# Performance work log

Hardware: AMD Instinct MI355X
Metric: run time of the kernel (lower is better)

## Reference

```python
import jax, jax.numpy as jnp
import numpy as np

N_NODES = 100000
N_RAND_EDGES = 1600000
NEG_SLOPE = 0.2


def setup_inputs() -> dict:
    key = jax.random.key(0)
    ks = jax.random.split(key, 12)
    X = jax.random.normal(ks[0], (N_NODES, 1433), dtype=jnp.float32)
    src_r = jax.random.randint(ks[1], (N_RAND_EDGES,), 0, N_NODES)
    dst_r = jax.random.randint(ks[2], (N_RAND_EDGES,), 0, N_NODES)
    loops = jnp.arange(N_NODES, dtype=src_r.dtype)
    src = jnp.concatenate([src_r, loops])  # [E] self loops ensure in-degree >= 1
    dst = jnp.concatenate([dst_r, loops])
    s0 = 1.0 / np.sqrt(1433.0)
    s1 = 1.0 / np.sqrt(140.0)
    W0 = jax.random.normal(ks[3], (1433, 140), jnp.float32) * s0
    al0 = jax.random.normal(ks[4], (140,), jnp.float32) * s1
    ar0 = jax.random.normal(ks[5], (140,), jnp.float32) * s1
    b0 = jnp.zeros((140,), jnp.float32)
    W1 = jax.random.normal(ks[6], (140, 7), jnp.float32) * s1
    al1 = jax.random.normal(ks[7], (7,), jnp.float32) * 0.3
    ar1 = jax.random.normal(ks[8], (7,), jnp.float32) * 0.3
    b1 = jnp.zeros((7,), jnp.float32)
    return dict(X=X, src=src, dst=dst, W0=W0, al0=al0, ar0=ar0, b0=b0,
                W1=W1, al1=al1, ar1=ar1, b1=b1)


def gat_layer(X, src, dst, W, al, ar, b):
    """One single-head DGL GATConv: proj -> edge attn -> edge softmax -> scatter -> bias -> ReLU."""
    n = X.shape[0]
    h = X @ W                      # [N, d_out]
    el = h @ al                    # [N] src attention term
    er = h @ ar                    # [N] dst attention term
    e = jax.nn.leaky_relu(el[src] + er[dst], NEG_SLOPE)   # [E]
    # segment softmax over incoming edges of each dst node
    m = jax.ops.segment_max(e, dst, num_segments=n)       # [N]
    ex = jnp.exp(e - m[dst])                              # [E]
    denom = jax.ops.segment_sum(ex, dst, num_segments=n)  # [N]
    a = ex / denom[dst]                                   # [E]
    msg = h[src] * a[:, None]                             # [E, d_out]
    out = jax.ops.segment_sum(msg, dst, num_segments=n)   # [N, d_out]
    return jax.nn.relu(out + b)


def reference(X, src, dst, W0, al0, ar0, b0, W1, al1, ar1, b1):
    h1 = gat_layer(X, src, dst, W0, al0, ar0, b0)   # [N, 140]
    h2 = gat_layer(h1, src, dst, W1, al1, ar1, b1)  # [N, 7]
    return h2
```

## Files before the change

kernel.cpp:

```cpp
#include <hip/hip_runtime.h>
#include <hip/hip_bf16.h>

typedef __bf16 bf16x8 __attribute__((ext_vector_type(8)));
typedef float f32x4 __attribute__((ext_vector_type(4)));
typedef unsigned short u16x8 __attribute__((ext_vector_type(8)));
typedef unsigned short ushort_t;

#define GK 1433
#define GN 140
#define NP 144
#define KT 45

__device__ __forceinline__ ushort_t f2bf_trunc(float v) {
    return (ushort_t)(__builtin_bit_cast(unsigned int, v) >> 16);
}
__device__ __forceinline__ ushort_t f2bf_rne(float v) {
    unsigned int u = __builtin_bit_cast(unsigned int, v);
    unsigned int r = u + 0x7fffu + ((u >> 16) & 1u);
    return (ushort_t)(r >> 16);
}
__device__ __forceinline__ float bf2f(unsigned int u16) {
    return __builtin_bit_cast(float, u16 << 16);
}

__global__ void k_wpack(const float* __restrict__ W0, ushort_t* __restrict__ Wp) {
    int i = blockIdx.x * 256 + threadIdx.x;
    if (i >= KT * 9 * 64) return;
    int lane = i & 63, tile = i >> 6;
    int kt = tile / 9, nt = tile - kt * 9;
    int n = nt * 16 + (lane & 15);
    int kb = kt * 32 + (lane >> 4) * 8;
    u16x8 v;
#pragma unroll
    for (int j = 0; j < 8; ++j) {
        int k = kb + j;
        v[j] = (k < GK && n < GN) ? f2bf_trunc(W0[k * GN + n]) : (ushort_t)0;
    }
    ((u16x8*)Wp)[i] = v;
}

__global__ __launch_bounds__(256) void k_gemm0(const float* __restrict__ X,
                                               const ushort_t* __restrict__ Wp,
                                               ushort_t* __restrict__ h0p, int M) {
    const int lane = threadIdx.x & 63;
    const int wave = threadIdx.x >> 6;
    const int m = lane & 15;
    const int q = lane >> 4;
    const int rowbase = blockIdx.x * 128 + wave * 32;

    f32x4 acc[2][9];
#pragma unroll
    for (int i = 0; i < 2; ++i)
#pragma unroll
        for (int j = 0; j < 9; ++j) acc[i][j] = (f32x4){0.f, 0.f, 0.f, 0.f};

    int r0 = rowbase + m;      if (r0 > M - 1) r0 = M - 1;
    int r1 = rowbase + 16 + m; if (r1 > M - 1) r1 = M - 1;
    const float* x0 = X + (size_t)r0 * GK;
    const float* x1 = X + (size_t)r1 * GK;
    const u16x8* wq = (const u16x8*)Wp;

    for (int kt = 0; kt < KT; ++kt) {
        const int kb = kt * 32 + q * 8;
        u16x8 t0, t1;
        if (kb + 8 <= GK) {
#pragma unroll
            for (int j = 0; j < 8; ++j) {
                t0[j] = f2bf_trunc(x0[kb + j]);
                t1[j] = f2bf_trunc(x1[kb + j]);
            }
        } else {
#pragma unroll
            for (int j = 0; j < 8; ++j) {
                int k = kb + j;
                t0[j] = (k < GK) ? f2bf_trunc(x0[k]) : (ushort_t)0;
                t1[j] = (k < GK) ? f2bf_trunc(x1[k]) : (ushort_t)0;
            }
        }
        bf16x8 a0 = __builtin_bit_cast(bf16x8, t0);
        bf16x8 a1 = __builtin_bit_cast(bf16x8, t1);
#pragma unroll
        for (int nt = 0; nt < 9; ++nt) {
            bf16x8 b = __builtin_bit_cast(bf16x8, wq[((kt * 9 + nt) << 6) + lane]);
            acc[0][nt] = __builtin_amdgcn_mfma_f32_16x16x32_bf16(a0, b, acc[0][nt], 0, 0, 0);
            acc[1][nt] = __builtin_amdgcn_mfma_f32_16x16x32_bf16(a1, b, acc[1][nt], 0, 0, 0);
        }
    }
#pragma unroll
    for (int mf = 0; mf < 2; ++mf)
#pragma unroll
        for (int reg = 0; reg < 4; ++reg) {
            int r = rowbase + mf * 16 + q * 4 + reg;
            if (r < M) {
                ushort_t* orow = h0p + (size_t)r * NP + m;
#pragma unroll
                for (int nt = 0; nt < 9; ++nt) orow[nt * 16] = f2bf_rne(acc[mf][nt][reg]);
            }
        }
}

__global__ __launch_bounds__(256) void k_elr0(const ushort_t* __restrict__ h0p,
                                              const float* __restrict__ al,
                                              const float* __restrict__ ar,
                                              float* __restrict__ el, float* __restrict__ er, int N) {
    __shared__ float als[NP], ars[NP];
    for (int i = threadIdx.x; i < NP; i += 256) {
        als[i] = (i < GN) ? al[i] : 0.f;
        ars[i] = (i < GN) ? ar[i] : 0.f;
    }
    __syncthreads();
    int node = blockIdx.x * 256 + threadIdx.x;
    if (node >= N) return;
    const unsigned int* row = (const unsigned int*)(h0p + (size_t)node * NP);
    float e1 = 0.f, e2 = 0.f;
#pragma unroll 4
    for (int f = 0; f < NP / 2; ++f) {
        unsigned int p = row[f];
        float v0 = bf2f(p & 0xffffu), v1 = bf2f(p >> 16);
        e1 += v0 * als[2 * f] + v1 * als[2 * f + 1];
        e2 += v0 * ars[2 * f] + v1 * ars[2 * f + 1];
    }
    el[node] = e1;
    er[node] = e2;
}

__global__ void k_hist(const int* __restrict__ dst, int E, int* __restrict__ counts) {
    int i = blockIdx.x * 256 + threadIdx.x;
    if (i < E) atomicAdd(&counts[dst[i]], 1);
}

__global__ void k_scan_block(const int* __restrict__ in, int n, int* __restrict__ part, int* __restrict__ bsum) {
    __shared__ int sh[256];
    int t = threadIdx.x, i = blockIdx.x * 256 + t;
    int v = (i < n) ? in[i] : 0;
    sh[t] = v;
    __syncthreads();
    for (int off = 1; off < 256; off <<= 1) {
        int add = (t >= off) ? sh[t - off] : 0;
        __syncthreads();
        sh[t] += add;
        __syncthreads();
    }
    if (i < n) part[i] = sh[t] - v;
    if (t == 255) bsum[blockIdx.x] = sh[255];
}

__global__ void k_scan_single(const int* __restrict__ in, int n, int* __restrict__ out) {
    __shared__ int sh[512];
    int t = threadIdx.x;
    int v = (t < n) ? in[t] : 0;
    sh[t] = v;
    __syncthreads();
    for (int off = 1; off < 512; off <<= 1) {
        int add = (t >= off) ? sh[t - off] : 0;
        __syncthreads();
        sh[t] += add;
        __syncthreads();
    }
    if (t < n) out[t] = sh[t] - v;
}

__global__ void k_offsets(const int* __restrict__ part, const int* __restrict__ bscan,
                          int N, int E, int* __restrict__ offsets) {
    int i = blockIdx.x * 256 + threadIdx.x;
    if (i < N) offsets[i] = part[i] + bscan[i >> 8];
    if (i == 0) offsets[N] = E;
}

__global__ void k_fill(const int* __restrict__ src, const int* __restrict__ dst, int E,
                       const int* __restrict__ offsets, int* __restrict__ cursor, int* __restrict__ eidx) {
    int i = blockIdx.x * 256 + threadIdx.x;
    if (i < E) {
        int d = dst[i];
        int p = atomicAdd(&cursor[d], 1);
        eidx[offsets[d] + p] = src[i];
    }
}

__device__ __forceinline__ float leaky(float x) { return (x > 0.f) ? x : 0.2f * x; }

__global__ __launch_bounds__(256) void k_agg0(const ushort_t* __restrict__ h0p,
                                              const float* __restrict__ el, const float* __restrict__ er,
                                              const int* __restrict__ offsets, const int* __restrict__ eidx,
                                              const float* __restrict__ b0,
                                              const float* __restrict__ W1,
                                              const float* __restrict__ al1,
                                              const float* __restrict__ ar1,
                                              float* __restrict__ h1p, float* __restrict__ el1,
                                              float* __restrict__ er1, int N) {
    __shared__ float W1s[NP * 8];
    __shared__ float b0s[NP];
    __shared__ float al1s[8], ar1s[8];
    int t = threadIdx.x;
    for (int i = t; i < NP * 8; i += 256) {
        int f = i >> 3, k = i & 7;
        W1s[i] = (f < GN && k < 7) ? W1[f * 7 + k] : 0.f;
    }
    for (int i = t; i < NP; i += 256) b0s[i] = (i < GN) ? b0[i] : 0.f;
    if (t < 8) {
        al1s[t] = (t < 7) ? al1[t] : 0.f;
        ar1s[t] = (t < 7) ? ar1[t] : 0.f;
    }
    __syncthreads();

    int node = blockIdx.x * 4 + (t >> 6);
    if (node >= N) return;
    int lane = t & 63;
    int s0 = offsets[node], s1 = offsets[node + 1];
    float erd = er[node];

    float mm = -1e30f;
    for (int j = s0 + lane; j < s1; j += 64) mm = fmaxf(mm, leaky(el[eidx[j]] + erd));
#pragma unroll
    for (int o = 1; o < 64; o <<= 1) mm = fmaxf(mm, __shfl_xor(mm, o));

    float dn = 0.f;
    for (int j = s0 + lane; j < s1; j += 64) dn += __expf(leaky(el[eidx[j]] + erd) - mm);
#pragma unroll
    for (int o = 1; o < 64; o <<= 1) dn += __shfl_xor(dn, o);
    float inv = 1.f / dn;

    float a0 = 0.f, a1 = 0.f, a2 = 0.f, a3 = 0.f;
    for (int j = s0; j < s1; ++j) {
        int s = eidx[j];
        float w = __expf(leaky(el[s] + erd) - mm) * inv;
        const unsigned int* hr = (const unsigned int*)(h0p + (size_t)s * NP);
        unsigned int pp = hr[lane];
        a0 += w * bf2f(pp & 0xffffu);
        a1 += w * bf2f(pp >> 16);
        if (lane < 8) {
            unsigned int pe = hr[64 + lane];
            a2 += w * bf2f(pe & 0xffffu);
            a3 += w * bf2f(pe >> 16);
        }
    }
    int f0 = 2 * lane, f1 = 2 * lane + 1;
    float h10 = fmaxf(a0 + b0s[f0], 0.f);
    float h11 = fmaxf(a1 + b0s[f1], 0.f);
    float h12 = 0.f, h13 = 0.f;
    if (lane < 8) {
        h12 = fmaxf(a2 + b0s[128 + 2 * lane], 0.f);
        h13 = fmaxf(a3 + b0s[129 + 2 * lane], 0.f);
    }

    float p[7];
#pragma unroll
    for (int k = 0; k < 7; ++k) {
        float v = h10 * W1s[f0 * 8 + k] + h11 * W1s[f1 * 8 + k];
        if (lane < 8) v += h12 * W1s[(128 + 2 * lane) * 8 + k] + h13 * W1s[(129 + 2 * lane) * 8 + k];
#pragma unroll
        for (int o = 1; o < 64; o <<= 1) v += __shfl_xor(v, o);
        p[k] = v;
    }
    if (lane == 0) {
        float e1 = 0.f, e2 = 0.f;
        float* hp = h1p + (size_t)node * 8;
#pragma unroll
        for (int k = 0; k < 7; ++k) {
            hp[k] = p[k];
            e1 += p[k] * al1s[k];
            e2 += p[k] * ar1s[k];
        }
        hp[7] = 0.f;
        el1[node] = e1;
        er1[node] = e2;
    }
}

__global__ __launch_bounds__(256) void k_agg1(const float* __restrict__ h1p,
                                              const float* __restrict__ el, const float* __restrict__ er,
                                              const int* __restrict__ offsets, const int* __restrict__ eidx,
                                              const float* __restrict__ b1,
                                              float* __restrict__ out, int N) {
    int t = threadIdx.x;
    int node = blockIdx.x * 4 + (t >> 6);
    if (node >= N) return;
    int lane = t & 63;
    int s0 = offsets[node], s1 = offsets[node + 1];
    float erd = er[node];

    float mm = -1e30f;
    for (int j = s0 + lane; j < s1; j += 64) mm = fmaxf(mm, leaky(el[eidx[j]] + erd));
#pragma unroll
    for (int o = 1; o < 64; o <<= 1) mm = fmaxf(mm, __shfl_xor(mm, o));

    float dn = 0.f;
    for (int j = s0 + lane; j < s1; j += 64) dn += __expf(leaky(el[eidx[j]] + erd) - mm);
#pragma unroll
    for (int o = 1; o < 64; o <<= 1) dn += __shfl_xor(dn, o);
    float inv = 1.f / dn;

    float acc[7] = {0.f, 0.f, 0.f, 0.f, 0.f, 0.f, 0.f};
    for (int j = s0 + lane; j < s1; j += 64) {
        int s = eidx[j];
        float w = __expf(leaky(el[s] + erd) - mm) * inv;
        const float4* hp = (const float4*)(h1p + (size_t)s * 8);
        float4 q0 = hp[0], q1 = hp[1];
        acc[0] += w * q0.x; acc[1] += w * q0.y; acc[2] += w * q0.z; acc[3] += w * q0.w;
        acc[4] += w * q1.x; acc[5] += w * q1.y; acc[6] += w * q1.z;
    }
#pragma unroll
    for (int k = 0; k < 7; ++k)
#pragma unroll
        for (int o = 1; o < 64; o <<= 1) acc[k] += __shfl_xor(acc[k], o);

    if (lane == 0) {
        float* orow = out + (size_t)node * 7;
#pragma unroll
        for (int k = 0; k < 7; ++k)
            orow[k] = fmaxf(acc[k] + b1[k], 0.f);
    }
}

extern "C" void kernel_launch(void* const* d_in, const int* in_sizes, int n_in,
                              void* d_out, int out_size, void* d_ws, size_t ws_size,
                              hipStream_t stream) {
    const float* X = (const float*)d_in[0];
    const int* src = (const int*)d_in[1];
    const int* dst = (const int*)d_in[2];
    const float* W0 = (const float*)d_in[3];
    const float* al0 = (const float*)d_in[4];
    const float* ar0 = (const float*)d_in[5];
    const float* b0 = (const float*)d_in[6];
    const float* W1 = (const float*)d_in[7];
    const float* al1 = (const float*)d_in[8];
    const float* ar1 = (const float*)d_in[9];
    const float* b1 = (const float*)d_in[10];
    float* out = (float*)d_out;

    const int N = in_sizes[0] / GK;
    const int E = in_sizes[1];

    char* w = (char*)d_ws;
    auto alloc = [&](size_t bytes) {
        char* p = w;
        w += (bytes + 255) & ~(size_t)255;
        return p;
    };
    ushort_t* wpack = (ushort_t*)alloc((size_t)KT * 9 * 64 * 8 * 2);
    ushort_t* h0p = (ushort_t*)alloc((size_t)N * NP * 2);
    float* el0 = (float*)alloc((size_t)N * 4);
    float* er0 = (float*)alloc((size_t)N * 4);
    int* counts = (int*)alloc(2 * (size_t)N * 4);
    int* cursor = counts + N;
    int* part = (int*)alloc((size_t)N * 4);
    int* bsum = (int*)alloc(512 * 4);
    int* bscan = (int*)alloc(512 * 4);
    int* offsets = (int*)alloc(((size_t)N + 1) * 4);
    int* eidx = (int*)alloc((size_t)E * 4);
    float* h1p = (float*)alloc((size_t)N * 8 * 4);
    float* el1 = (float*)alloc((size_t)N * 4);
    float* er1 = (float*)alloc((size_t)N * 4);

    hipMemsetAsync(counts, 0, 2 * (size_t)N * sizeof(int), stream);

    k_wpack<<<(KT * 9 * 64 + 255) / 256, 256, 0, stream>>>(W0, wpack);
    k_gemm0<<<(N + 127) / 128, 256, 0, stream>>>(X, wpack, h0p, N);
    k_elr0<<<(N + 255) / 256, 256, 0, stream>>>(h0p, al0, ar0, el0, er0, N);

    int nb = (N + 255) / 256;
    k_hist<<<(E + 255) / 256, 256, 0, stream>>>(dst, E, counts);
    k_scan_block<<<nb, 256, 0, stream>>>(counts, N, part, bsum);
    k_scan_single<<<1, 512, 0, stream>>>(bsum, nb, bscan);
    k_offsets<<<nb, 256, 0, stream>>>(part, bscan, N, E, offsets);
    k_fill<<<(E + 255) / 256, 256, 0, stream>>>(src, dst, E, offsets, cursor, eidx);

    k_agg0<<<(N + 3) / 4, 256, 0, stream>>>(h0p, el0, er0, offsets, eidx, b0, W1, al1, ar1,
                                            h1p, el1, er1, N);
    k_agg1<<<(N + 3) / 4, 256, 0, stream>>>(h1p, el1, er1, offsets, eidx, b1, out, N);
}
```

Baseline: 1.463 ms.

## Fuse attention logits into GEMM epilogue and add single-pass small-degree softmax aggregation

Computes el/er for layer 0 in the GEMM epilogue from the fp32 accumulators using 16-lane shuffles, which removes the separate k_elr0 kernel and its re-read of h0. For nodes with in-degree up to 64, both aggregation kernels now load each edge's source index and logit once per lane, do the softmax with wave reductions, and broadcast index and weight via readlane. This replaces three passes over eidx/el, and layer 0 unrolls the gather by two edges. Row padding grows from 144 to 160 so the tail loads with lane&7 stay in bounds, at the cost of more h0 storage and bandwidth. El/er are now taken from fp32 values rather than the bf16-rounded h0, which changes numerics slightly.

Result: faster. 1.317 ms (-10.0%).

```diff
diff --git a/kernel.cpp b/kernel.cpp
--- a/kernel.cpp
+++ b/kernel.cpp
@@ -8,7 +8,7 @@
 
 #define GK 1433
 #define GN 140
-#define NP 144
+#define NP 160
 #define KT 45
 
 __device__ __forceinline__ ushort_t f2bf_trunc(float v) {
@@ -21,6 +21,9 @@
 }
 __device__ __forceinline__ float bf2f(unsigned int u16) {
     return __builtin_bit_cast(float, u16 << 16);
+}
+__device__ __forceinline__ float bcast_f(float v, int lane) {
+    return __builtin_bit_cast(float, __builtin_amdgcn_readlane(__builtin_bit_cast(int, v), lane));
 }
 
 __global__ void k_wpack(const float* __restrict__ W0, ushort_t* __restrict__ Wp) {
@@ -41,7 +44,11 @@
 
 __global__ __launch_bounds__(256) void k_gemm0(const float* __restrict__ X,
                                                const ushort_t* __restrict__ Wp,
-                                               ushort_t* __restrict__ h0p, int M) {
+                                               const float* __restrict__ al0,
+                                               const float* __restrict__ ar0,
+                                               ushort_t* __restrict__ h0p,
+                                               float* __restrict__ el, float* __restrict__ er,
+                                               int M) {
     const int lane = threadIdx.x & 63;
     const int wave = threadIdx.x >> 6;
     const int m = lane & 15;
@@ -86,6 +93,7 @@
             acc[1][nt] = __builtin_amdgcn_mfma_f32_16x16x32_bf16(a1, b, acc[1][nt], 0, 0, 0);
         }
     }
+
 #pragma unroll
     for (int mf = 0; mf < 2; ++mf)
 #pragma unroll
@@ -97,31 +105,36 @@
                 for (int nt = 0; nt < 9; ++nt) orow[nt * 16] = f2bf_rne(acc[mf][nt][reg]);
             }
         }
-}
-
-__global__ __launch_bounds__(256) void k_elr0(const ushort_t* __restrict__ h0p,
-                                              const float* __restrict__ al,
-                                              const float* __restrict__ ar,
-                                              float* __restrict__ el, float* __restrict__ er, int N) {
-    __shared__ float als[NP], ars[NP];
-    for (int i = threadIdx.x; i < NP; i += 256) {
-        als[i] = (i < GN) ? al[i] : 0.f;
-        ars[i] = (i < GN) ? ar[i] : 0.f;
-    }
-    __syncthreads();
-    int node = blockIdx.x * 256 + threadIdx.x;
-    if (node >= N) return;
-    const unsigned int* row = (const unsigned int*)(h0p + (size_t)node * NP);
-    float e1 = 0.f, e2 = 0.f;
-#pragma unroll 4
-    for (int f = 0; f < NP / 2; ++f) {
-        unsigned int p = row[f];
-        float v0 = bf2f(p & 0xffffu), v1 = bf2f(p >> 16);
-        e1 += v0 * als[2 * f] + v1 * als[2 * f + 1];
-        e2 += v0 * ars[2 * f] + v1 * ars[2 * f + 1];
-    }
-    el[node] = e1;
-    er[node] = e2;
+
+    float alv[9], arv[9];
+#pragma unroll
+    for (int nt = 0; nt < 9; ++nt) {
+        int c = nt * 16 + m;
+        alv[nt] = (c < GN) ? al0[c] : 0.f;
+        arv[nt] = (c < GN) ? ar0[c] : 0.f;
+    }
+#pragma unroll
+    for (int mf = 0; mf < 2; ++mf)
+#pragma unroll
+        for (int reg = 0; reg < 4; ++reg) {
+            float e1 = 0.f, e2 = 0.f;
+#pragma unroll
+            for (int nt = 0; nt < 9; ++nt) {
+                float v = acc[mf][nt][reg];
+                e1 += v * alv[nt];
+                e2 += v * arv[nt];
+            }
+#pragma unroll
+            for (int o = 1; o < 16; o <<= 1) {
+                e1 += __shfl_xor(e1, o);
+                e2 += __shfl_xor(e2, o);
+            }
+            int r = rowbase + mf * 16 + q * 4 + reg;
+            if (m == 0 && r < M) {
+                el[r] = e1;
+                er[r] = e2;
+            }
+        }
 }
 
 __global__ void k_hist(const int* __restrict__ dst, int E, int* __restrict__ counts) {
@@ -207,33 +220,78 @@
     if (node >= N) return;
     int lane = t & 63;
     int s0 = offsets[node], s1 = offsets[node + 1];
+    int deg = s1 - s0;
     float erd = er[node];
 
-    float mm = -1e30f;
-    for (int j = s0 + lane; j < s1; j += 64) mm = fmaxf(mm, leaky(el[eidx[j]] + erd));
-#pragma unroll
-    for (int o = 1; o < 64; o <<= 1) mm = fmaxf(mm, __shfl_xor(mm, o));
-
-    float dn = 0.f;
-    for (int j = s0 + lane; j < s1; j += 64) dn += __expf(leaky(el[eidx[j]] + erd) - mm);
-#pragma unroll
-    for (int o = 1; o < 64; o <<= 1) dn += __shfl_xor(dn, o);
-    float inv = 1.f / dn;
-
     float a0 = 0.f, a1 = 0.f, a2 = 0.f, a3 = 0.f;
-    for (int j = s0; j < s1; ++j) {
-        int s = eidx[j];
-        float w = __expf(leaky(el[s] + erd) - mm) * inv;
-        const unsigned int* hr = (const unsigned int*)(h0p + (size_t)s * NP);
-        unsigned int pp = hr[lane];
-        a0 += w * bf2f(pp & 0xffffu);
-        a1 += w * bf2f(pp >> 16);
-        if (lane < 8) {
-            unsigned int pe = hr[64 + lane];
+
+    if (deg <= 64) {
+        int sj = 0;
+        float ej = -1e30f;
+        if (lane < deg) {
+            sj = eidx[s0 + lane];
+            ej = leaky(el[sj] + erd);
+        }
+        float mm = ej;
+#pragma unroll
+        for (int o = 1; o < 64; o <<= 1) mm = fmaxf(mm, __shfl_xor(mm, o));
+        float pj = __expf(ej - mm);
+        float dn = pj;
+#pragma unroll
+        for (int o = 1; o < 64; o <<= 1) dn += __shfl_xor(dn, o);
+        float wj = pj * (1.f / dn);
+
+        int j = 0;
+        for (; j + 1 < deg; j += 2) {
+            int sa = __builtin_amdgcn_readlane(sj, j);
+            int sb = __builtin_amdgcn_readlane(sj, j + 1);
+            float wa = bcast_f(wj, j);
+            float wb = bcast_f(wj, j + 1);
+            const unsigned int* ha = (const unsigned int*)(h0p + (size_t)sa * NP);
+            const unsigned int* hb = (const unsigned int*)(h0p + (size_t)sb * NP);
+            unsigned int pa = ha[lane], pb = hb[lane];
+            unsigned int ea = ha[64 + (lane & 7)], eb = hb[64 + (lane & 7)];
+            a0 += wa * bf2f(pa & 0xffffu) + wb * bf2f(pb & 0xffffu);
+            a1 += wa * bf2f(pa >> 16) + wb * bf2f(pb >> 16);
+            a2 += wa * bf2f(ea & 0xffffu) + wb * bf2f(eb & 0xffffu);
+            a3 += wa * bf2f(ea >> 16) + wb * bf2f(eb >> 16);
+        }
+        if (j < deg) {
+            int sa = __builtin_amdgcn_readlane(sj, j);
+            float wa = bcast_f(wj, j);
+            const unsigned int* ha = (const unsigned int*)(h0p + (size_t)sa * NP);
+            unsigned int pa = ha[lane];
+            unsigned int ea = ha[64 + (lane & 7)];
+            a0 += wa * bf2f(pa & 0xffffu);
+            a1 += wa * bf2f(pa >> 16);
+            a2 += wa * bf2f(ea & 0xffffu);
+            a3 += wa * bf2f(ea >> 16);
+        }
+    } else {
+        float mm = -1e30f;
+        for (int j = s0 + lane; j < s1; j += 64) mm = fmaxf(mm, leaky(el[eidx[j]] + erd));
+#pragma unroll
+        for (int o = 1; o < 64; o <<= 1) mm = fmaxf(mm, __shfl_xor(mm, o));
+
+        float dn = 0.f;
+        for (int j = s0 + lane; j < s1; j += 64) dn += __expf(leaky(el[eidx[j]] + erd) - mm);
+#pragma unroll
+        for (int o = 1; o < 64; o <<= 1) dn += __shfl_xor(dn, o);
+        float inv = 1.f / dn;
+
+        for (int j = s0; j < s1; ++j) {
+            int s = eidx[j];
+            float w = __expf(leaky(el[s] + erd) - mm) * inv;
+            const unsigned int* hr = (const unsigned int*)(h0p + (size_t)s * NP);
+            unsigned int pp = hr[lane];
+            unsigned int pe = hr[64 + (lane & 7)];
+            a0 += w * bf2f(pp & 0xffffu);
+            a1 += w * bf2f(pp >> 16);
             a2 += w * bf2f(pe & 0xffffu);
             a3 += w * bf2f(pe >> 16);
         }
     }
+
     int f0 = 2 * lane, f1 = 2 * lane + 1;
     float h10 = fmaxf(a0 + b0s[f0], 0.f);
     float h11 = fmaxf(a1 + b0s[f1], 0.f);
@@ -277,28 +335,55 @@
     if (node >= N) return;
     int lane = t & 63;
     int s0 = offsets[node], s1 = offsets[node + 1];
+    int deg = s1 - s0;
     float erd = er[node];
 
-    float mm = -1e30f;
-    for (int j = s0 + lane; j < s1; j += 64) mm = fmaxf(mm, leaky(el[eidx[j]] + erd));
-#pragma unroll
-    for (int o = 1; o < 64; o <<= 1) mm = fmaxf(mm, __shfl_xor(mm, o));
-
-    float dn = 0.f;
-    for (int j = s0 + lane; j < s1; j += 64) dn += __expf(leaky(el[eidx[j]] + erd) - mm);
-#pragma unroll
-    for (int o = 1; o < 64; o <<= 1) dn += __shfl_xor(dn, o);
-    float inv = 1.f / dn;
-
     float acc[7] = {0.f, 0.f, 0.f, 0.f, 0.f, 0.f, 0.f};
-    for (int j = s0 + lane; j < s1; j += 64) {
-        int s = eidx[j];
-        float w = __expf(leaky(el[s] + erd) - mm) * inv;
-        const float4* hp = (const float4*)(h1p + (size_t)s * 8);
-        float4 q0 = hp[0], q1 = hp[1];
-        acc[0] += w * q0.x; acc[1] += w * q0.y; acc[2] += w * q0.z; acc[3] += w * q0.w;
-        acc[4] += w * q1.x; acc[5] += w * q1.y; acc[6] += w * q1.z;
-    }
+
+    if (deg <= 64) {
+        int sj = 0;
+        float ej = -1e30f;
+        if (lane < deg) {
+            sj = eidx[s0 + lane];
+            ej = leaky(el[sj] + erd);
+        }
+        float mm = ej;
+#pragma unroll
+        for (int o = 1; o < 64; o <<= 1) mm = fmaxf(mm, __shfl_xor(mm, o));
+        float pj = __expf(ej - mm);
+        float dn = pj;
+#pragma unroll
+        for (int o = 1; o < 64; o <<= 1) dn += __shfl_xor(dn, o);
+        float wj = pj * (1.f / dn);
+
+        if (lane < deg) {
+            const float4* hp = (const float4*)(h1p + (size_t)sj * 8);
+            float4 q0 = hp[0], q1 = hp[1];
+            acc[0] = wj * q0.x; acc[1] = wj * q0.y; acc[2] = wj * q0.z; acc[3] = wj * q0.w;
+            acc[4] = wj * q1.x; acc[5] = wj * q1.y; acc[6] = wj * q1.z;
+        }
+    } else {
+        float mm = -1e30f;
+        for (int j = s0 + lane; j < s1; j += 64) mm = fmaxf(mm, leaky(el[eidx[j]] + erd));
+#pragma unroll
+        for (int o = 1; o < 64; o <<= 1) mm = fmaxf(mm, __shfl_xor(mm, o));
+
+        float dn = 0.f;
+        for (int j = s0 + lane; j < s1; j += 64) dn += __expf(leaky(el[eidx[j]] + erd) - mm);
+#pragma unroll
+        for (int o = 1; o < 64; o <<= 1) dn += __shfl_xor(dn, o);
+        float inv = 1.f / dn;
+
+        for (int j = s0 + lane; j < s1; j += 64) {
+            int s = eidx[j];
+            float w = __expf(leaky(el[s] + erd) - mm) * inv;
+            const float4* hp = (const float4*)(h1p + (size_t)s * 8);
+            float4 q0 = hp[0], q1 = hp[1];
+            acc[0] += w * q0.x; acc[1] += w * q0.y; acc[2] += w * q0.z; acc[3] += w * q0.w;
+            acc[4] += w * q1.x; acc[5] += w * q1.y; acc[6] += w * q1.z;
+        }
+    }
+
 #pragma unroll
     for (int k = 0; k < 7; ++k)
 #pragma unroll
@@ -355,8 +440,7 @@
     hipMemsetAsync(counts, 0, 2 * (size_t)N * sizeof(int), stream);
 
     k_wpack<<<(KT * 9 * 64 + 255) / 256, 256, 0, stream>>>(W0, wpack);
-    k_gemm0<<<(N + 127) / 128, 256, 0, stream>>>(X, wpack, h0p, N);
-    k_elr0<<<(N + 255) / 256, 256, 0, stream>>>(h0p, al0, ar0, el0, er0, N);
+    k_gemm0<<<(N + 127) / 128, 256, 0, stream>>>(X, wpack, al0, ar0, h0p, el0, er0, N);
 
     int nb = (N + 255) / 256;
     k_hist<<<(E + 255) / 256, 256, 0, stream>>>(dst, E, counts);
```
